# Kernel optimization log

Measured on AMD Instinct MI355X. Metric: run time of the kernel, lower is better.

## Reference

```python
import jax, jax.numpy as jnp
import numpy as np
from jax import lax

E = 10        # embed_dim
SEQ = 4000    # input_frame (sample_length=40)
G = 800       # group
F = 5         # frames_in_group
B = 16
VOCAB = 8192


def _conv2d(x, w, b):
    # x: [B, C, H, W], w: [O, I, 3, 3], padding=1 -> SAME
    y = lax.conv_general_dilated(x, w, (1, 1), 'SAME',
                                 dimension_numbers=('NCHW', 'OIHW', 'NCHW'))
    return y + b[None, :, None, None]


def _conv1d_k1(x, w, b):
    # Conv1d(seq, seq, kernel=1): x [B, S, L], w [S_out, S_in]
    return jnp.einsum('oi,bil->bol', w, x) + b[None, :, None]


def _linear(x, w, b):
    # torch Linear: w [out, in]
    return x @ w.T + b


def setup_inputs() -> dict:
    key = jax.random.key(0)
    ks = jax.random.split(key, 24)
    s = 0.02
    inp = {
        'X': jax.random.randint(ks[0], (B, SEQ, 15), 0, VOCAB),
        'emb_table': jax.random.normal(ks[1], (VOCAB, E), jnp.float32),
        'w_dwc_lsp': jax.random.normal(ks[2], (G, G, 3, 3), jnp.float32) * s,
        'b_dwc_lsp': jnp.zeros((G,), jnp.float32),
        'w_dwc_other': jax.random.normal(ks[3], (G, G, 3, 3), jnp.float32) * s,
        'b_dwc_other': jnp.zeros((G,), jnp.float32),
        'w_local': jax.random.normal(ks[4], (SEQ, SEQ), jnp.float32) * s,
        'b_local': jnp.zeros((SEQ,), jnp.float32),
        'w_global': jax.random.normal(ks[5], (SEQ, SEQ), jnp.float32) * s,
        'b_global': jnp.zeros((SEQ,), jnp.float32),
        'w_gq': jax.random.normal(ks[6], (4 * E, 4 * E), jnp.float32) * s,
        'b_gq': jnp.zeros((4 * E,), jnp.float32),
        'w_cq': jax.random.normal(ks[7], (4 * E, 4 * E), jnp.float32) * s,
        'b_cq': jnp.zeros((4 * E,), jnp.float32),
        'w_pq': jax.random.normal(ks[8], (4 * E, 3 * E), jnp.float32) * s,
        'b_pq': jnp.zeros((4 * E,), jnp.float32),
        'w_lk': jax.random.normal(ks[9], (4 * E, 4 * E), jnp.float32) * s,
        'b_lk': jnp.zeros((4 * E,), jnp.float32),
        'w_lv': jax.random.normal(ks[10], (4 * E, 4 * E), jnp.float32) * s,
        'b_lv': jnp.zeros((4 * E,), jnp.float32),
        'w_cls': jax.random.normal(ks[11], (1, SEQ * 4 * E * 3), jnp.float32) * 0.001,
        'b_cls': jnp.zeros((1,), jnp.float32),
        'bn_w': jnp.ones((1,), jnp.float32),
        'bn_b': jnp.zeros((1,), jnp.float32),
    }
    return inp


def reference(X, emb_table, w_dwc_lsp, b_dwc_lsp, w_dwc_other, b_dwc_other,
              w_local, b_local, w_global, b_global,
              w_gq, b_gq, w_cq, b_cq, w_pq, b_pq,
              w_lk, b_lk, w_lv, b_lv, w_cls, b_cls, bn_w, bn_b):
    batch, seq, cw = X.shape
    gamma = jnp.float32(0.8)
    pk = jnp.array([0, 0, 0, 0, 1, 3, 1, 2, 3, 2, 3, 1, 2, 3, 3], jnp.float32)
    D = jnp.repeat(gamma ** pk, E)  # [150]

    Xe = emb_table[X].reshape(batch, seq, cw * E) * D  # [B, S, 150]
    ch = Xe.reshape(batch, seq, cw, E)                  # 15 chunks of E

    lsp = ch[:, :, jnp.array([0, 1, 2, 3])].reshape(batch, seq, 4 * E)
    pitch = ch[:, :, jnp.array([4, 5, 10])].reshape(batch, seq, 3 * E)
    code = ch[:, :, jnp.array([6, 7, 11, 12])].reshape(batch, seq, 4 * E)
    gain = ch[:, :, jnp.array([8, 13, 9, 14])].reshape(batch, seq, 4 * E)

    conv_lsp = _conv2d(lsp.reshape(batch, G, F, 4 * E), w_dwc_lsp, b_dwc_lsp).reshape(batch, seq, 4 * E)
    conv_pitch = _conv2d(pitch.reshape(batch, G, F, 3 * E), w_dwc_other, b_dwc_other).reshape(batch, seq, 3 * E)
    conv_code = _conv2d(code.reshape(batch, G, F, 4 * E), w_dwc_other, b_dwc_other).reshape(batch, seq, 4 * E)
    conv_gain = _conv2d(gain.reshape(batch, G, F, 4 * E), w_dwc_other, b_dwc_other).reshape(batch, seq, 4 * E)

    conv_lsp = _conv1d_k1(conv_lsp, w_local, b_local)
    conv_pitch = _conv1d_k1(conv_pitch, w_local, b_local)
    conv_code = _conv1d_k1(conv_code, w_local, b_local)
    conv_gain = _conv1d_k1(conv_gain, w_local, b_local)

    gain_q = _linear(conv_gain, w_gq, b_gq)    # [B, S, 40]
    pitch_q = _linear(conv_pitch, w_pq, b_pq)  # [B, S, 40]
    code_q = _linear(conv_code, w_cq, b_cq)    # [B, S, 40]
    lsp_k = _linear(conv_lsp, w_lk, b_lk)
    lsp_v = _linear(conv_lsp, w_lv, b_lv)

    # Q @ K^T @ V with no softmax: associate as Q @ (K^T V), O(S*d^2)
    kv = jnp.einsum('bsd,bse->bde', lsp_k, lsp_v)  # [B, 40, 40]
    out_gain = jnp.einsum('bsd,bde->bse', gain_q, kv) + lsp
    out_pitch = jnp.einsum('bsd,bde->bse', pitch_q, kv) + lsp
    out_code = jnp.einsum('bsd,bde->bse', code_q, kv) + lsp

    atten_out = jnp.concatenate([out_gain, out_pitch, out_code], -1)  # [B, S, 120]
    gf = _conv1d_k1(atten_out, w_global, b_global).reshape(batch, -1)  # [B, 480000]

    y = gf @ w_cls.T + b_cls  # [B, 1]
    # BatchNorm1d(1) in eval mode: running_mean=0, running_var=1
    eps = jnp.float32(1e-5)
    y = y * (bn_w / jnp.sqrt(1.0 + eps)) + bn_b
    return jax.nn.sigmoid(y)
```

## Files before the change

### kernel.cpp

```cpp
#include <hip/hip_runtime.h>
#include <hip/hip_bf16.h>

typedef _Float16 f16;
typedef __attribute__((ext_vector_type(8))) _Float16 half8;
typedef __attribute__((ext_vector_type(4))) _Float16 half4;
typedef __attribute__((ext_vector_type(4))) float f32x4;

static const int BN = 16, SEQN = 4000;

__device__ __forceinline__ void gload_lds(f16* lds, const f16* g) {
  __builtin_amdgcn_global_load_lds((const __attribute__((address_space(1))) unsigned int*)g,
                                   (__attribute__((address_space(3))) unsigned int*)lds, 16, 0, 0);
}

__device__ __forceinline__ int xcd_swz(int orig, int nwg) {
  int q = nwg >> 3, r = nwg & 7, x = orig & 7, o = orig >> 3;
  return (x < r ? x * (q + 1) : r * (q + 1) + (x - r) * q) + o;
}

__device__ __forceinline__ void body_wconv(char* SM, int o,
    const float* __restrict__ w_dwc_l, f16* __restrict__ wp_lsp) {
  float* sh = (float*)SM;
  int t = threadIdx.x;
  for (int p4 = t; p4 < 1800; p4 += 256)
    *(f32x4*)&sh[p4 * 4] = *(const f32x4*)&w_dwc_l[(long)o * 7200 + p4 * 4];
  __syncthreads();
  for (int c = t; c < 912; c += 256) {
    int p = c * 8;
    int seg = p / 2432, r = p - seg * 2432;
    half8 h = {};
    if (r < 2400) {
      int de = r / 800, gib = r - de * 800;
#pragma unroll
      for (int j = 0; j < 8; j++) h[j] = (f16)sh[(gib + j) * 9 + seg * 3 + de];
    }
    *(half8*)&wp_lsp[(long)o * 7296 + p] = h;
  }
}

__device__ __forceinline__ void body_wlocal(char* SM, int s,
    const float* __restrict__ w_local, f16* __restrict__ wlp) {
  float* sh = (float*)SM;
  int t = threadIdx.x;
  for (int p4 = t; p4 < 1000; p4 += 256)
    *(f32x4*)&sh[p4 * 4] = *(const f32x4*)&w_local[(long)s * 4000 + p4 * 4];
  __syncthreads();
  for (int c = t; c < 512; c += 256) {
    int p = c * 8;
    half8 h = {};
    if (p < 4000) {
      int f = p / 800, g = p - f * 800;
#pragma unroll
      for (int j = 0; j < 8; j++) h[j] = (f16)sh[(g + j) * 5 + f];
    }
    *(half8*)&wlp[(long)s * 4096 + p] = h;
  }
}

__device__ __forceinline__ void body_wcT(char* SM, int id,
    const float* __restrict__ w_cls, f16* __restrict__ wcT) {
  float (*tile)[33] = (float(*)[33])SM;
  int t = threadIdx.x;
  int c0 = (id % 4) * 32, r0 = (id / 4) * 32;
  int tx = t & 31, ty = t >> 5;
  for (int i = ty; i < 32; i += 8) {
    int r = r0 + i, c = c0 + tx;
    tile[i][tx] = (r < 4000 && c < 120) ? w_cls[(long)r * 120 + c] : 0.f;
  }
  __syncthreads();
  for (int i = ty; i < 32; i += 8) {
    int c = c0 + i, r = r0 + tx;
    if (c < 128 && r < 4000) wcT[(long)c * 4000 + r] = (f16)(tile[tx][i] * 1024.f);
  }
}

__device__ __forceinline__ void body_woT(char* SM, int id,
    const float* __restrict__ in, f16* __restrict__ out) {
  float (*sh)[292] = (float(*)[292])SM;
  int bg = id % 25, bgi = id / 25;
  int g0 = bg * 32, gi0 = bgi * 32;
  int t = threadIdx.x;
  for (int p = t; p < 2304; p += 256) {
    int gl = p / 72, q4 = p % 72;
    *(f32x4*)&sh[gl][q4 * 4] = *(const f32x4*)&in[(long)(g0 + gl) * 7200 + gi0 * 9 + q4 * 4];
  }
  __syncthreads();
  for (int c = t; c < 1152; c += 256) {
    int gl8 = c & 3, q = c >> 2;
    int gil = q & 31, z = q >> 5;
    half8 h;
#pragma unroll
    for (int j = 0; j < 8; j++) h[j] = (f16)sh[gl8 * 8 + j][gil * 9 + z];
    *(half8*)&out[(long)z * 640000 + (gi0 + gil) * 800 + g0 + gl8 * 8] = h;
  }
}

__device__ __forceinline__ void body_gather(char* SM, int bid,
    const int* __restrict__ X, const float* __restrict__ emb,
    f16* __restrict__ P_lsp, f16* __restrict__ P_pit,
    f16* __restrict__ P_cod, f16* __restrict__ P_gai,
    float* __restrict__ lsp32) {
  int* sx_ = (int*)SM;
  float* slsp = (float*)(SM + 9600);
  const float scale[15] = {1.f,1.f,1.f,1.f,0.8f,0.512f,0.8f,0.64f,0.512f,0.64f,0.512f,0.8f,0.64f,0.512f,0.512f};
  const int br[15] = {0,0,0,0,1,1,2,2,3,3,1,2,2,3,3};
  const int po[15] = {0,1,2,3,0,1,0,1,0,2,2,2,3,1,3};
  int t = threadIdx.x;
  int b = bid / 25, gc = bid % 25;
  int g0 = gc * 32, s0 = g0 * 5;
  const int* xbase = X + ((long)b * SEQN + s0) * 15;
  for (int p = t; p < 600; p += 256)
    *(f32x4*)&sx_[p * 4] = *(const f32x4*)&xbase[p * 4];
  __syncthreads();
  for (int it = t; it < 2400; it += 256) {
    int gl = it & 31, q = it >> 5, f = q % 5, c = q / 5;
    int idx = sx_[(gl * 5 + f) * 15 + c];
    const float* er = emb + (long)idx * 10;
    int ty = br[c], p = po[c];
    f16* P = (ty == 0) ? P_lsp : (ty == 1) ? P_pit : (ty == 2) ? P_cod : P_gai;
    int Wp = (ty == 1) ? 32 : 42;
    f16* base = P + ((long)((f + 1) * 16 + b) * Wp + (1 + p * 10)) * 800 + g0 + gl;
    float sc = scale[c];
#pragma unroll
    for (int j = 0; j < 10; j++) {
      float v = er[j] * sc;
      base[(long)j * 800] = (f16)v;
      if (ty == 0) slsp[(gl * 5 + f) * 40 + p * 10 + j] = v;
    }
  }
  __syncthreads();
  float* ldst = lsp32 + ((long)b * SEQN + s0) * 40;
  for (int p4 = t; p4 < 1600; p4 += 256)
    *(f32x4*)&ldst[p4 * 4] = *(const f32x4*)&slsp[p4 * 4];
}

__device__ __forceinline__ void body_c1(char* SM, int blk,
    const float* __restrict__ wcls, const float* __restrict__ bg,
    float* __restrict__ c1p) {
  float* red = (float*)SM;
  int t = threadIdx.x;
  float s = 0.f;
  for (long i = (long)blk * 256 + t; i < 480000; i += (long)120 * 256)
    s += wcls[i] * bg[i / 120];
  red[t] = s; __syncthreads();
  for (int o = 128; o > 0; o >>= 1) { if (t < o) red[t] += red[t + o]; __syncthreads(); }
  if (t == 0) c1p[blk] = red[0];
}

__device__ __forceinline__ void body_conv(char* SM, int id,
    const f16* __restrict__ P, const f16* __restrict__ wp, float* __restrict__ Cp) {
  f16* Asb = (f16*)SM;
  f16* Bsb = Asb + 8192;
  int lin = xcd_swz(id % 175, 175);
  int z = id / 175;
  int nx = lin % 7, my = lin / 7;
  int m0 = my * 128, n0 = nx * 128;
  Cp += (long)z * 3200 * 800;
  int t = threadIdx.x;
  int gslot = (t & 3) ^ ((t >> 3) & 3);
  const f16 *ap[2], *bp[2];
#pragma unroll
  for (int q = 0; q < 2; q++) {
    int row = q * 64 + (t >> 2);
    int m = m0 + row;
    int f = m / 640, rem = m % 640, b = rem / 40, e = rem % 40;
    ap[q] = P + ((long)((f + z) * 16 + b) * 42 + e) * 800 + gslot * 8;
    bp[q] = wp + (long)(n0 + row) * 7296 + z * 2432 + gslot * 8;
  }
  int lane = t & 63, wv = t >> 6, l15 = lane & 15, kg = lane >> 4;
  int wm = (wv >> 1) * 64, wn = (wv & 1) * 64;
  int so = (kg ^ ((l15 >> 1) & 3)) << 3;
  f32x4 acc[4][4] = {};
  gload_lds(&Asb[t * 8], ap[0]); gload_lds(&Asb[2048 + t * 8], ap[1]);
  gload_lds(&Bsb[t * 8], bp[0]); gload_lds(&Bsb[2048 + t * 8], bp[1]);
  __syncthreads();
  int cur = 0;
  for (int kt = 0; kt < 76; kt++) {
    if (kt + 1 < 76) {
      int o = (kt + 1) * 32, nb = cur ^ 1;
      gload_lds(&Asb[nb * 4096 + t * 8], ap[0] + o); gload_lds(&Asb[nb * 4096 + 2048 + t * 8], ap[1] + o);
      gload_lds(&Bsb[nb * 4096 + t * 8], bp[0] + o); gload_lds(&Bsb[nb * 4096 + 2048 + t * 8], bp[1] + o);
    }
    half8 av[4], bv[4];
#pragma unroll
    for (int i = 0; i < 4; i++) av[i] = *(const half8*)&Asb[cur * 4096 + (wm + i * 16 + l15) * 32 + so];
#pragma unroll
    for (int j = 0; j < 4; j++) bv[j] = *(const half8*)&Bsb[cur * 4096 + (wn + j * 16 + l15) * 32 + so];
#pragma unroll
    for (int i = 0; i < 4; i++)
#pragma unroll
      for (int j = 0; j < 4; j++)
        acc[i][j] = __builtin_amdgcn_mfma_f32_16x16x32_f16(av[i], bv[j], acc[i][j], 0, 0, 0);
    __syncthreads();
    cur ^= 1;
  }
#pragma unroll
  for (int i = 0; i < 4; i++) {
    int mb = m0 + wm + i * 16 + kg * 4;
#pragma unroll
    for (int j = 0; j < 4; j++) {
      int n = n0 + wn + j * 16 + l15;
      if (n >= 800) continue;
      f32x4 d = acc[i][j];
#pragma unroll
      for (int r = 0; r < 4; r++)
        Cp[(long)(mb + r) * 800 + n] = d[r];
    }
  }
}

__device__ __forceinline__ void body_gemm128(char* SM, int x, int ky, int z,
    const f16* __restrict__ A, int lda, const f16* __restrict__ Bm, int ldb,
    float* __restrict__ C, int ldc,
    int gx, int nwg, int nkt, int KTtot, long cslice, long az, long bz, long cz,
    int Mreal, int Nreal, int Aclamp) {
  f16* Asb = (f16*)SM;
  f16* Bsb = Asb + 8192;
  A += (long)z * az;
  Bm += (long)z * bz;
  C += (long)z * cz + (long)ky * cslice;
  int lin = xcd_swz(x, nwg);
  int nx = lin % gx, my = lin / gx;
  int m0 = my * 128, n0 = nx * 128;
  int kt0 = ky * nkt;
  int ktn = nkt; if (kt0 + ktn > KTtot) ktn = KTtot - kt0;
  int t = threadIdx.x;
  int gslot = (t & 3) ^ ((t >> 3) & 3);
  const f16 *ap[2], *bp[2];
#pragma unroll
  for (int q = 0; q < 2; q++) {
    int row = q * 64 + (t >> 2);
    int ra = m0 + row; if (ra >= Aclamp) ra = Aclamp - 1;
    ap[q] = A + (long)ra * lda + (long)kt0 * 32 + gslot * 8;
    bp[q] = Bm + (long)(n0 + row) * ldb + (long)kt0 * 32 + gslot * 8;
  }
  int lane = t & 63, wv = t >> 6, l15 = lane & 15, kg = lane >> 4;
  int wm = (wv >> 1) * 64, wn = (wv & 1) * 64;
  int so = (kg ^ ((l15 >> 1) & 3)) << 3;
  f32x4 acc[4][4] = {};
  gload_lds(&Asb[t * 8], ap[0]); gload_lds(&Asb[2048 + t * 8], ap[1]);
  gload_lds(&Bsb[t * 8], bp[0]); gload_lds(&Bsb[2048 + t * 8], bp[1]);
  __syncthreads();
  int cur = 0;
  for (int kt = 0; kt < ktn; kt++) {
    if (kt + 1 < ktn) {
      int o = (kt + 1) * 32, nb = cur ^ 1;
      gload_lds(&Asb[nb * 4096 + t * 8], ap[0] + o); gload_lds(&Asb[nb * 4096 + 2048 + t * 8], ap[1] + o);
      gload_lds(&Bsb[nb * 4096 + t * 8], bp[0] + o); gload_lds(&Bsb[nb * 4096 + 2048 + t * 8], bp[1] + o);
    }
    half8 av[4], bv[4];
#pragma unroll
    for (int i = 0; i < 4; i++) av[i] = *(const half8*)&Asb[cur * 4096 + (wm + i * 16 + l15) * 32 + so];
#pragma unroll
    for (int j = 0; j < 4; j++) bv[j] = *(const half8*)&Bsb[cur * 4096 + (wn + j * 16 + l15) * 32 + so];
#pragma unroll
    for (int i = 0; i < 4; i++)
#pragma unroll
      for (int j = 0; j < 4; j++)
        acc[i][j] = __builtin_amdgcn_mfma_f32_16x16x32_f16(av[i], bv[j], acc[i][j], 0, 0, 0);
    __syncthreads();
    cur ^= 1;
  }
#pragma unroll
  for (int i = 0; i < 4; i++) {
    int mb = m0 + wm + i * 16 + kg * 4;
#pragma unroll
    for (int j = 0; j < 4; j++) {
      int n = n0 + wn + j * 16 + l15;
      if (n >= Nreal) continue;
      f32x4 d = acc[i][j];
#pragma unroll
      for (int r = 0; r < 4; r++) {
        int m = mb + r;
        if (m >= Mreal) continue;
        C[(long)m * ldc + n] = d[r];
      }
    }
  }
}

__device__ __forceinline__ void body_tn(char* SM, int id,
    const f16* __restrict__ A, int lda, const float* __restrict__ B, int ldb,
    float* __restrict__ C, int ldc, int nkt, int KTtot, long cslice,
    int Mreal, int Nreal) {
  f16* As = (f16*)SM;
  f16* Bs = As + 4096;
  int n0 = (id & 31) * 128;
  int ky = id >> 5;
  int kt0 = ky * nkt;
  int ktn = nkt; if (kt0 + ktn > KTtot) ktn = KTtot - kt0;
  C += (long)ky * cslice;
  int t = threadIdx.x;
  int gslot = (t & 3) ^ ((t >> 3) & 3);
  const f16 *ap0, *ap1;
  {
    int r0 = t >> 2, r1 = 64 + (t >> 2);
    if (r0 >= Mreal) r0 = Mreal - 1;
    if (r1 >= Mreal) r1 = Mreal - 1;
    ap0 = A + (long)r0 * lda + (long)kt0 * 32 + gslot * 8;
    ap1 = A + (long)r1 * lda + (long)kt0 * 32 + gslot * 8;
  }
  int lane = t & 63, wv = t >> 6;
  int wm = (wv >> 1) * 64, wn = (wv & 1) * 64;
  int l15 = lane & 15, kg = lane >> 4;
  int so = (kg ^ ((l15 >> 1) & 3)) << 3;
  f32x4 acc[4][4] = {};
  for (int kt = 0; kt < ktn; kt++) {
    float rb[4][4];
    int nli[4], kqi[4];
#pragma unroll
    for (int i = 0; i < 4; i++) {
      int idd = i * 256 + t;
      nli[i] = idd & 127; kqi[i] = idd >> 7;
      int gn = n0 + nli[i]; if (gn >= Nreal) gn = Nreal - 1;
      long kb = ((long)(kt0 + kt) * 32 + kqi[i] * 4);
#pragma unroll
      for (int j = 0; j < 4; j++) rb[i][j] = B[(kb + j) * ldb + gn];
    }
    __syncthreads();
    gload_lds(&As[t * 8], ap0 + kt * 32);
    gload_lds(&As[2048 + t * 8], ap1 + kt * 32);
#pragma unroll
    for (int i = 0; i < 4; i++) {
      half4 h = {(f16)rb[i][0], (f16)rb[i][1], (f16)rb[i][2], (f16)rb[i][3]};
      *(half4*)&Bs[nli[i] * 36 + kqi[i] * 4] = h;
    }
    __syncthreads();
    half8 av[4], bv[4];
#pragma unroll
    for (int i = 0; i < 4; i++) {
      av[i] = *(const half8*)(&As[(wm + i * 16 + l15) * 32 + so]);
      bv[i] = *(const half8*)(&Bs[(wn + i * 16 + l15) * 36 + kg * 8]);
    }
#pragma unroll
    for (int i = 0; i < 4; i++)
#pragma unroll
      for (int j = 0; j < 4; j++)
        acc[i][j] = __builtin_amdgcn_mfma_f32_16x16x32_f16(av[i], bv[j], acc[i][j], 0, 0, 0);
  }
#pragma unroll
  for (int i = 0; i < 4; i++) {
    int mb = wm + i * 16 + kg * 4;
#pragma unroll
    for (int j = 0; j < 4; j++) {
      int n = n0 + wn + j * 16 + l15;
      if (n >= Nreal) continue;
      f32x4 d = acc[i][j];
#pragma unroll
      for (int r = 0; r < 4; r++) {
        int m = mb + r;
        if (m >= Mreal) continue;
        C[(long)m * ldc + n] = d[r];
      }
    }
  }
}

__device__ __forceinline__ void body_co_red(long gid,
    const float* __restrict__ Cp, const float* __restrict__ bias, f16* __restrict__ co) {
  if (gid >= 640000) return;
  int m = gid / 200, n4 = (gid % 200) * 4;
  long o = (long)m * 800 + n4;
  f32x4 s = *(const f32x4*)&bias[n4];
#pragma unroll
  for (int z = 0; z < 3; z++) s += *(const f32x4*)&Cp[(long)z * 2560000 + o];
  int f = m / 640, r2 = m % 640;
  half4 h = {(f16)s[0], (f16)s[1], (f16)s[2], (f16)s[3]};
  *(half4*)&co[(long)r2 * 4000 + f * 800 + n4] = h;
}

__device__ __forceinline__ void body_vred(int idb, int MODE,
    const float* __restrict__ vp, float* __restrict__ vout, f16* __restrict__ tout) {
  int x = idb & 15, ec = idb >> 4;
  int s = x * 256 + threadIdx.x;
  if (s >= 4000) return;
  int g = s / 5, f = s % 5;
  float sums[40];
#pragma unroll
  for (int eo = 0; eo < 40; eo++) {
    int e = ec * 40 + eo;
    float sum = 0.f;
#pragma unroll
    for (int z = 0; z < 10; z++) sum += vp[(long)z * 480000 + (long)e * 4000 + s];
    sums[eo] = sum;
    if (MODE == 0) tout[(long)e * 4000 + s] = (f16)sum;
    else tout[(long)(f * 120 + e) * 832 + g] = (f16)sum;
  }
#pragma unroll
  for (int q = 0; q < 10; q++)
    *(f32x4*)&vout[(long)s * 120 + ec * 40 + q * 4] = *(f32x4*)&sums[q * 4];
}

__device__ __forceinline__ void body_cl_red(long gid,
    const float* __restrict__ Clp, const float* __restrict__ bl, float* __restrict__ cl) {
  if (gid >= 640000) return;
  int m = gid / 160, n4 = (gid % 160) * 4;
  long o = (long)m * 640 + n4;
  f32x4 s = {0.f, 0.f, 0.f, 0.f};
#pragma unroll
  for (int z = 0; z < 4; z++) s += *(const f32x4*)&Clp[(long)z * 2560000 + o];
  float b = bl[m];
  s += (f32x4){b, b, b, b};
  *(f32x4*)&cl[o] = s;
}

__device__ __forceinline__ void body_resid(char* SM, int chunk, int b,
    const float* __restrict__ lsp32, const float* __restrict__ vmat,
    float* __restrict__ rpart) {
  float* red = (float*)SM;
  int t = threadIdx.x;
  int s0 = chunk * 160;
  float y = 0.f;
  for (int idx = t; idx < 1600; idx += 256) {
    int sr = idx / 10, d4 = idx % 10;
    const float* lp = lsp32 + ((long)b * SEQN + s0 + sr) * 40 + d4 * 4;
    const float* vp = vmat + (long)(s0 + sr) * 120 + d4 * 4;
    f32x4 l = *(const f32x4*)lp;
    f32x4 vs = *(const f32x4*)vp + *(const f32x4*)(vp + 40) + *(const f32x4*)(vp + 80);
    y += l[0] * vs[0] + l[1] * vs[1] + l[2] * vs[2] + l[3] * vs[3];
  }
  red[t] = y; __syncthreads();
  for (int o = 128; o > 0; o >>= 1) { if (t < o) red[t] += red[t + o]; __syncthreads(); }
  if (t == 0) rpart[b * 25 + chunk] = red[0];
}

__device__ __forceinline__ void body_kv(char* SM, int chunk, int b,
    const float* __restrict__ cl, const float* __restrict__ wlk, const float* __restrict__ blk,
    const float* __restrict__ wlv, const float* __restrict__ blv, float* __restrict__ kvp) {
  float* s_wk = (float*)SM;
  float* s_wv = s_wk + 1600;
  float* s_cl = s_wv + 1600;
  float* s_k  = s_cl + 320;
  float* s_v  = s_k + 320;
  int t = threadIdx.x;
  for (int p = t; p < 1600; p += 256) { s_wk[p] = wlk[p]; s_wv[p] = wlv[p]; }
  float acc[7] = {0.f, 0.f, 0.f, 0.f, 0.f, 0.f, 0.f};
  for (int c8 = 0; c8 < 20; c8++) {
    int sb = chunk * 160 + c8 * 8;
    __syncthreads();
    for (int p = t; p < 320; p += 256) {
      int sl = p / 40, e = p % 40;
      s_cl[sl * 40 + e] = cl[(long)(sb + sl) * 640 + b * 40 + e];
    }
    __syncthreads();
    for (int p = t; p < 640; p += 256) {
      int half = p / 320, q = p % 320, sl = q / 40, d = q % 40;
      const float* w = half ? s_wv : s_wk;
      float r = half ? blv[d] : blk[d];
      for (int e = 0; e < 40; e++) r += w[d * 40 + e] * s_cl[sl * 40 + e];
      if (half) s_v[sl * 40 + d] = r; else s_k[sl * 40 + d] = r;
    }
    __syncthreads();
    int ai = 0;
    for (int p = t; p < 1600; p += 256, ai++) {
      int d = p / 40, e = p % 40;
      float a = acc[ai];
      for (int sl = 0; sl < 8; sl++) a += s_k[sl * 40 + d] * s_v[sl * 40 + e];
      acc[ai] = a;
    }
  }
  int ai = 0;
  for (int p = t; p < 1600; p += 256, ai++)
    kvp[((long)(b * 25 + chunk)) * 1600 + p] = acc[ai];
}

__device__ __forceinline__ void body_consts(char* SM, int e,
    const float* __restrict__ Vt, const float* __restrict__ vmat,
    const float* __restrict__ bconv, const float* __restrict__ blocal,
    float* __restrict__ cbblv, float* __restrict__ svv) {
  float* r1 = (float*)SM;
  float* r2 = r1 + 256;
  int t = threadIdx.x;
  float a = 0.f, b = 0.f;
  for (int s = t; s < 4000; s += 256) {
    a += bconv[s / 5] * Vt[(long)s * 120 + e] + blocal[s] * vmat[(long)s * 120 + e];
    b += vmat[(long)s * 120 + e];
  }
  r1[t] = a; r2[t] = b; __syncthreads();
  for (int o = 128; o > 0; o >>= 1) {
    if (t < o) { r1[t] += r1[t + o]; r2[t] += r2[t + o]; }
    __syncthreads();
  }
  if (t == 0) { cbblv[e] = r1[0]; svv[e] = r2[0]; }
}

__device__ __forceinline__ void body_fold(long c8,
    const float* __restrict__ A9, f16* __restrict__ Bp) {
  long p = c8 * 8;
  if (p >= 7 * 120 * 2496) return;
  int fp = p / 299520;
  int r = p % 299520;
  int eg = r / 2496, k2 = r % 2496;
  int zk = k2 / 832, kk = k2 % 832;
  half8 h = {};
  if (kk < 800) {
#pragma unroll
    for (int j = 0; j < 8; j++) {
      float s = 0.f;
#pragma unroll
      for (int dh = 0; dh < 3; dh++) {
        int f = fp - dh;
        if (f >= 0 && f < 5)
          s += A9[((long)(dh * 3 + zk) * 640 + f * 120 + eg) * 800 + kk + j];
      }
      h[j] = (f16)s;
    }
  }
  *(half8*)&Bp[p] = h;
}

__device__ __forceinline__ void body_kvred(long gid,
    const float* __restrict__ kvp, float* __restrict__ kv) {
  if (gid >= 16 * 1600) return;
  int b = gid / 1600, p = gid % 1600;
  float s = 0.f;
  for (int c = 0; c < 25; c++) s += kvp[((long)(b * 25 + c)) * 1600 + p];
  kv[gid] = s;
}

__device__ __forceinline__ void body_U(char* SM, int id,
    const f16* __restrict__ Pg, const f16* __restrict__ Pp, const f16* __restrict__ Pc,
    const f16* __restrict__ Bp, float* __restrict__ Upart) {
  f16* Asb = (f16*)SM;
  f16* Bsb = Asb + 8192;
  int m0 = (id % 28) * 64;
  int y = id / 28, fp = y / 3, zk = y % 3;
  const f16* P; int seg0, jw, Wp, e0;
  if (m0 < 640)       { seg0 = 0;    jw = 40; Wp = 42; e0 = 0;  P = Pg; }
  else if (m0 < 1152) { seg0 = 640;  jw = 30; Wp = 32; e0 = 40; P = Pp; }
  else                { seg0 = 1152; jw = 40; Wp = 42; e0 = 80; P = Pc; }
  P += (long)fp * 16 * Wp * 800;
  int t = threadIdx.x;
  int gslot = (t & 7) ^ ((t >> 3) & 7);
  const f16 *ap[2], *bp[2];
#pragma unroll
  for (int q = 0; q < 2; q++) {
    int row = q * 32 + (t >> 3);
    int l = m0 + row - seg0; if (l >= 16 * jw) l = 0;
    ap[q] = P + ((long)(l / jw) * Wp + (l % jw)) * 800 + (long)zk * 800 + gslot * 8;
    int brow = row; if (e0 + brow > 119) brow = 119 - e0;
    bp[q] = Bp + ((long)fp * 120 + e0 + brow) * 2496 + zk * 832 + gslot * 8;
  }
  int lane = t & 63, wv = t >> 6, l15 = lane & 15, kg = lane >> 4;
  int sx = l15 & 7;
  f32x4 acc[3] = {};
  gload_lds(&Asb[t * 8], ap[0]); gload_lds(&Asb[2048 + t * 8], ap[1]);
  gload_lds(&Bsb[t * 8], bp[0]); gload_lds(&Bsb[2048 + t * 8], bp[1]);
  __syncthreads();
  int cur = 0;
  for (int kt = 0; kt < 13; kt++) {
    if (kt + 1 < 13) {
      int o = (kt + 1) * 64, nb = cur ^ 1;
      gload_lds(&Asb[nb * 4096 + t * 8], ap[0] + o); gload_lds(&Asb[nb * 4096 + 2048 + t * 8], ap[1] + o);
      gload_lds(&Bsb[nb * 4096 + t * 8], bp[0] + o); gload_lds(&Bsb[nb * 4096 + 2048 + t * 8], bp[1] + o);
    }
#pragma unroll
    for (int ks = 0; ks < 2; ks++) {
      int so = ((ks * 4 + kg) ^ sx) << 3;
      half8 av = *(const half8*)&Asb[cur * 4096 + (wv * 16 + l15) * 64 + so];
#pragma unroll
      for (int j = 0; j < 3; j++) {
        half8 bv = *(const half8*)&Bsb[cur * 4096 + (j * 16 + l15) * 64 + so];
        acc[j] = __builtin_amdgcn_mfma_f32_16x16x32_f16(av, bv, acc[j], 0, 0, 0);
      }
    }
    __syncthreads();
    cur ^= 1;
  }
#pragma unroll
  for (int j = 0; j < 3; j++) {
    int n = j * 16 + l15;
    if (n >= 40) continue;
    f32x4 d = acc[j];
#pragma unroll
    for (int r = 0; r < 4; r++) {
      int m = m0 + wv * 16 + kg * 4 + r;
      if (m - seg0 >= 16 * jw) continue;
      Upart[((long)y * 1792 + m) * 40 + n] = d[r];
    }
  }
}

__device__ __forceinline__ void body_ured(long gid,
    const float* __restrict__ Upart, const float* __restrict__ cbblv,
    float* __restrict__ Ufin) {
  if (gid >= 1792 * 40) return;
  int m = gid / 40, e = gid % 40;
  int e0 = m < 640 ? 0 : (m < 1152 ? 40 : 80);
  float s = cbblv[e0 + e];
  for (int y = 0; y < 21; y++) s += Upart[(long)y * 71680 + gid];
  Ufin[gid] = s;
}

__global__ __launch_bounds__(256) void k_phase0(
    const float* w_dwc_l, f16* wp_lsp, const float* w_cls, f16* wcT,
    const int* X, const float* emb, f16* P_lsp, f16* P_pit, f16* P_cod, f16* P_gai,
    float* lsp32, const float* b_global, float* c1p) {
  __shared__ __align__(16) char SM[35200];
  int bid = blockIdx.x;
  if (bid < 800) body_wconv(SM, bid, w_dwc_l, wp_lsp);
  else if (bid < 1300) body_wcT(SM, bid - 800, w_cls, wcT);
  else if (bid < 1700) body_gather(SM, bid - 1300, X, emb, P_lsp, P_pit, P_cod, P_gai, lsp32);
  else body_c1(SM, bid - 1700, w_cls, b_global, c1p);
}

__global__ __launch_bounds__(256) void k_phase1(
    const f16* P_lsp, const f16* wp_lsp, float* Cp,
    const f16* wcT, const float* w_global, float* vpart,
    const float* w_local, f16* wlp) {
  __shared__ __align__(16) char SM[32768];
  int bid = blockIdx.x;
  if (bid < 525) body_conv(SM, bid, P_lsp, wp_lsp, Cp);
  else if (bid < 845) body_tn(SM, bid - 525, wcT, 4000, w_global, 4000, vpart, 4000, 13, 125, 480000L, 120, 4000);
  else body_wlocal(SM, bid - 845, w_local, wlp);
}

__global__ __launch_bounds__(256) void k_phase2(
    const float* Cp, const float* b_dwc_l, f16* co,
    const float* vpart, float* vmat, f16* vT,
    const float* w_dwc_o, f16* woT) {
  __shared__ __align__(16) char SM[37376];
  int bid = blockIdx.x;
  if (bid < 2500) body_co_red((long)bid * 256 + threadIdx.x, Cp, b_dwc_l, co);
  else if (bid < 2548) body_vred(bid - 2500, 0, vpart, vmat, vT);
  else body_woT(SM, bid - 2548, w_dwc_o, woT);
}

__global__ __launch_bounds__(256) void k_phase3(
    const f16* wlp, const f16* co, float* Clp,
    const f16* vT, const float* w_local, float* vpart,
    const float* lsp32, const float* vmat, float* rpart) {
  __shared__ __align__(16) char SM[32768];
  int bid = blockIdx.x;
  if (bid < 640) body_gemm128(SM, bid % 160, bid / 160, 0, wlp, 4096, co, 4000, Clp, 640,
                              5, 160, 32, 128, 2560000L, 0, 0, 0, 4000, 640, 4000);
  else if (bid < 960) body_tn(SM, bid - 640, vT, 4000, w_local, 4000, vpart, 4000, 13, 125, 480000L, 120, 4000);
  else { int id = bid - 960; body_resid(SM, id % 25, id / 25, lsp32, vmat, rpart); }
}

__global__ __launch_bounds__(256) void k_phase4(
    const float* Clp, const float* b_local, float* cl,
    const float* vpart, float* Vt, f16* vtT) {
  int bid = blockIdx.x;
  if (bid < 2500) body_cl_red((long)bid * 256 + threadIdx.x, Clp, b_local, cl);
  else body_vred(bid - 2500, 1, vpart, Vt, vtT);
}

__global__ __launch_bounds__(256) void k_phase5(
    const float* cl, const float* w_lk, const float* b_lk,
    const float* w_lv, const float* b_lv, float* kvp,
    const f16* vtT, const f16* woT, float* A9,
    const float* Vt, const float* vmat, const float* b_dwc_o, const float* b_local,
    float* cbblv, float* svv) {
  __shared__ __align__(16) char SM[32768];
  int bid = blockIdx.x;
  if (bid < 400) body_kv(SM, bid % 25, bid / 25, cl, w_lk, b_lk, w_lv, b_lv, kvp);
  else if (bid < 715) { int id = bid - 400; body_gemm128(SM, id % 35, 0, id / 35, vtT, 832, woT, 800, A9, 800,
                                                          7, 35, 26, 26, 0L, 0, 640000, 512000, 600, 800, 600); }
  else body_consts(SM, bid - 715, Vt, vmat, b_dwc_o, b_local, cbblv, svv);
}

__global__ __launch_bounds__(256) void k_phase6(
    const float* A9, f16* Bp, const float* kvp, float* kvb) {
  int bid = blockIdx.x;
  if (bid < 1024) body_fold((long)bid * 256 + threadIdx.x, A9, Bp);
  else body_kvred((long)(bid - 1024) * 256 + threadIdx.x, kvp, kvb);
}

__global__ __launch_bounds__(256) void k_phase7(
    const f16* P_gai, const f16* P_pit, const f16* P_cod,
    const f16* Bp, float* Upart) {
  __shared__ __align__(16) char SM[32768];
  body_U(SM, blockIdx.x, P_gai, P_pit, P_cod, Bp, Upart);
}

__global__ __launch_bounds__(256) void k_phase8(
    const float* Upart, const float* cbblv, float* Ufin) {
  body_ured((long)blockIdx.x * 256 + threadIdx.x, Upart, cbblv, Ufin);
}

__global__ __launch_bounds__(256) void k_final(
    const float* __restrict__ Ufin, const float* __restrict__ kvb,
    const float* __restrict__ rpart,
    const float* __restrict__ wgq, const float* __restrict__ wpq, const float* __restrict__ wcq,
    const float* __restrict__ bgq, const float* __restrict__ bpq, const float* __restrict__ bcq,
    const float* __restrict__ svv, const float* __restrict__ c1p,
    const float* __restrict__ bcls, const float* __restrict__ bnw,
    const float* __restrict__ bnb, float* __restrict__ out) {
  __shared__ float s_kv[1600], s_U[4800], s_w[4400], s_bq[120], s_sv[120], s_red[256];
  int b = blockIdx.x, t = threadIdx.x;
  for (int p = t; p < 1600; p += 256) {
    s_kv[p] = kvb[b * 1600 + p];
    s_w[p] = wgq[p];
    s_w[2800 + p] = wcq[p];
  }
  for (int p = t; p < 1200; p += 256) s_w[1600 + p] = wpq[p];
  for (int p = t; p < 4800; p += 256) {
    int tt = p / 1600, r = p % 1600, j = r / 40, e = r % 40;
    float uv = 0.f;
    if (tt == 0) uv = Ufin[(b * 40 + j) * 40 + e];
    else if (tt == 1) { if (j < 30) uv = Ufin[(640 + b * 30 + j) * 40 + e]; }
    else uv = Ufin[(1152 + b * 40 + j) * 40 + e];
    s_U[p] = uv;
  }
  if (t < 40) { s_bq[t] = bgq[t]; s_bq[40 + t] = bpq[t]; s_bq[80 + t] = bcq[t]; }
  for (int p = t; p < 120; p += 256) s_sv[p] = svv[p];
  __syncthreads();
  float y = 0.f;
  for (int p = t; p < 4800; p += 256) {
    int tt = p / 1600, q = p % 1600, d = q / 40, e = q % 40;
    float T = 0.f;
    if (tt == 0) {
      for (int j = 0; j < 40; j++) T += s_w[d * 40 + j] * s_U[j * 40 + e];
    } else if (tt == 1) {
      for (int j = 0; j < 30; j++) T += s_w[1600 + d * 30 + j] * s_U[1600 + j * 40 + e];
    } else {
      for (int j = 0; j < 40; j++) T += s_w[2800 + d * 40 + j] * s_U[3200 + j * 40 + e];
    }
    y += s_kv[d * 40 + e] * (T + s_bq[tt * 40 + d] * s_sv[tt * 40 + e]);
  }
  for (int p = t; p < 25; p += 256) y += rpart[b * 25 + p];
  s_red[t] = y; __syncthreads();
  for (int o = 128; o > 0; o >>= 1) { if (t < o) s_red[t] += s_red[t + o]; __syncthreads(); }
  if (t == 0) {
    float c1 = bcls[0];
    for (int i = 0; i < 120; i++) c1 += c1p[i];
    float yy = s_red[0] * (1.f / 1024.f) + c1;
    yy = yy * (bnw[0] * rsqrtf(1.f + 1e-5f)) + bnb[0];
    out[b] = 1.f / (1.f + expf(-yy));
  }
}

extern "C" void kernel_launch(void* const* d_in, const int* in_sizes, int n_in,
                              void* d_out, int out_size, void* d_ws, size_t ws_size,
                              hipStream_t stream) {
  const int*   X        = (const int*)d_in[0];
  const float* emb      = (const float*)d_in[1];
  const float* w_dwc_l  = (const float*)d_in[2];
  const float* b_dwc_l  = (const float*)d_in[3];
  const float* w_dwc_o  = (const float*)d_in[4];
  const float* b_dwc_o  = (const float*)d_in[5];
  const float* w_local  = (const float*)d_in[6];
  const float* b_local  = (const float*)d_in[7];
  const float* w_global = (const float*)d_in[8];
  const float* b_global = (const float*)d_in[9];
  const float* w_gq = (const float*)d_in[10];
  const float* b_gq = (const float*)d_in[11];
  const float* w_cq = (const float*)d_in[12];
  const float* b_cq = (const float*)d_in[13];
  const float* w_pq = (const float*)d_in[14];
  const float* b_pq = (const float*)d_in[15];
  const float* w_lk = (const float*)d_in[16];
  const float* b_lk = (const float*)d_in[17];
  const float* w_lv = (const float*)d_in[18];
  const float* b_lv = (const float*)d_in[19];
  const float* w_cls = (const float*)d_in[20];
  const float* b_cls = (const float*)d_in[21];
  const float* bn_w = (const float*)d_in[22];
  const float* bn_b = (const float*)d_in[23];
  float* out = (float*)d_out;

  char* ws = (char*)d_ws;
  size_t off = 0;
  auto alloc = [&](size_t bytes) -> void* {
    off = (off + 255) & ~(size_t)255;
    void* p = ws + off; off += bytes; return p;
  };

  const size_t sz_p40 = (size_t)7 * 16 * 42 * 800 * 2;
  const size_t sz_p30 = (size_t)7 * 16 * 32 * 800 * 2;
  f16* P_lsp = (f16*)alloc(sz_p40 + 256);
  f16* P_pit = (f16*)alloc(sz_p30 + 256);
  f16* P_cod = (f16*)alloc(sz_p40 + 256);
  f16* P_gai = (f16*)alloc(sz_p40 + 256);
  float* lsp32 = (float*)alloc((size_t)16 * 4000 * 40 * 4);
  f16* wp_lsp = (f16*)alloc((size_t)896 * 7296 * 2);
  f16* wlp    = (f16*)alloc((size_t)4000 * 4096 * 2 + 256);
  f16* wcT    = (f16*)alloc((size_t)128 * 4000 * 2);
  f16* vT     = (f16*)alloc((size_t)128 * 4000 * 2);
  f16* co     = (f16*)alloc((size_t)640 * 4000 * 2 + 256);
  float* cl   = (float*)alloc((size_t)4000 * 640 * 4);
  float* vmat  = (float*)alloc((size_t)480000 * 4);
  float* Vt    = (float*)alloc((size_t)480000 * 4);
  f16* vtT   = (f16*)alloc((size_t)640 * 832 * 2 + 256);
  f16* Bp    = (f16*)alloc((size_t)7 * 120 * 2496 * 2);
  float* Upart = (float*)alloc((size_t)21 * 1792 * 40 * 4);
  float* Ufin  = (float*)alloc((size_t)1792 * 40 * 4);
  float* cbblv = (float*)alloc(120 * 4);
  float* svv   = (float*)alloc(120 * 4);
  float* kvp  = (float*)alloc((size_t)400 * 1600 * 4);
  float* kvb  = (float*)alloc((size_t)16 * 1600 * 4);
  float* c1p  = (float*)alloc(120 * 4);
  float* rpart = (float*)alloc(400 * 4);
  f16* woT = (f16*)alloc(((size_t)9 * 640000 + 76800) * 2);
  float* vpart = (float*)alloc((size_t)10 * 480000 * 4);
  char* arena = (char*)alloc((size_t)41 * 1024 * 1024);
  float* Cp  = (float*)arena;
  float* Clp = (float*)arena;
  float* A9  = (float*)arena;
  (void)ws_size; (void)in_sizes; (void)n_in; (void)out_size;

  hipMemsetAsync(P_lsp, 0, sz_p40, stream);
  hipMemsetAsync(P_pit, 0, sz_p30, stream);
  hipMemsetAsync(P_cod, 0, sz_p40, stream);
  hipMemsetAsync(P_gai, 0, sz_p40, stream);
  hipMemsetAsync(vtT, 0, (size_t)640 * 832 * 2, stream);

  k_phase0<<<1820, 256, 0, stream>>>(w_dwc_l, wp_lsp, w_cls, wcT,
                                     X, emb, P_lsp, P_pit, P_cod, P_gai,
                                     lsp32, b_global, c1p);
  k_phase1<<<4845, 256, 0, stream>>>(P_lsp, wp_lsp, Cp, wcT, w_global, vpart,
                                     w_local, wlp);
  k_phase2<<<3173, 256, 0, stream>>>(Cp, b_dwc_l, co, vpart, vmat, vT, w_dwc_o, woT);
  k_phase3<<<1360, 256, 0, stream>>>(wlp, co, Clp, vT, w_local, vpart, lsp32, vmat, rpart);
  k_phase4<<<2548, 256, 0, stream>>>(Clp, b_local, cl, vpart, Vt, vtT);
  k_phase5<<<835, 256, 0, stream>>>(cl, w_lk, b_lk, w_lv, b_lv, kvp,
                                    vtT, woT, A9, Vt, vmat, b_dwc_o, b_local, cbblv, svv);
  k_phase6<<<1124, 256, 0, stream>>>(A9, Bp, kvp, kvb);
  k_phase7<<<588, 256, 0, stream>>>(P_gai, P_pit, P_cod, Bp, Upart);
  k_phase8<<<280, 256, 0, stream>>>(Upart, cbblv, Ufin);
  k_final<<<16, 256, 0, stream>>>(Ufin, kvb, rpart,
                                  w_gq, w_pq, w_cq, b_gq, b_pq, b_cq,
                                  svv, c1p, b_cls, bn_w, bn_b, out);
}
```

Before: 456.0 us.

## Split conv K into halves with fp16 partials and fp16 local-conv partials

The conv GEMM's K range per tap is split into two halves, so twice as many blocks run, each with half the k-loop. The reduction kernel now sums six partials instead of three. Both the conv and local-GEMM partial outputs are stored as fp16 instead of fp32, halving partial-buffer traffic and shrinking the arena. The w_local repack also stages data in a transposed LDS layout so the readback is contiguous. This trades some accuracy (fp16 partial sums) and extra reduction reads for more parallelism and less memory traffic.

```diff
diff --git a/kernel.cpp b/kernel.cpp
--- a/kernel.cpp
+++ b/kernel.cpp
@@ -42,16 +42,19 @@
     const float* __restrict__ w_local, f16* __restrict__ wlp) {
   float* sh = (float*)SM;
   int t = threadIdx.x;
-  for (int p4 = t; p4 < 1000; p4 += 256)
-    *(f32x4*)&sh[p4 * 4] = *(const f32x4*)&w_local[(long)s * 4000 + p4 * 4];
+  for (int p = t; p < 4000; p += 256) {
+    int g = p / 5, f = p - g * 5;
+    sh[f * 808 + g] = w_local[(long)s * 4000 + p];
+  }
   __syncthreads();
   for (int c = t; c < 512; c += 256) {
     int p = c * 8;
     half8 h = {};
     if (p < 4000) {
       int f = p / 800, g = p - f * 800;
-#pragma unroll
-      for (int j = 0; j < 8; j++) h[j] = (f16)sh[(g + j) * 5 + f];
+      const float* src = &sh[f * 808 + g];
+#pragma unroll
+      for (int j = 0; j < 8; j++) h[j] = (f16)src[j];
     }
     *(half8*)&wlp[(long)s * 4096 + p] = h;
   }
@@ -148,14 +151,15 @@
 }
 
 __device__ __forceinline__ void body_conv(char* SM, int id,
-    const f16* __restrict__ P, const f16* __restrict__ wp, float* __restrict__ Cp) {
+    const f16* __restrict__ P, const f16* __restrict__ wp, f16* __restrict__ Cp) {
   f16* Asb = (f16*)SM;
   f16* Bsb = Asb + 8192;
   int lin = xcd_swz(id % 175, 175);
   int z = id / 175;
+  int df = z >> 1, hf = z & 1;
   int nx = lin % 7, my = lin / 7;
   int m0 = my * 128, n0 = nx * 128;
-  Cp += (long)z * 3200 * 800;
+  Cp += (long)z * 2560000;
   int t = threadIdx.x;
   int gslot = (t & 3) ^ ((t >> 3) & 3);
   const f16 *ap[2], *bp[2];
@@ -164,8 +168,8 @@
     int row = q * 64 + (t >> 2);
     int m = m0 + row;
     int f = m / 640, rem = m % 640, b = rem / 40, e = rem % 40;
-    ap[q] = P + ((long)((f + z) * 16 + b) * 42 + e) * 800 + gslot * 8;
-    bp[q] = wp + (long)(n0 + row) * 7296 + z * 2432 + gslot * 8;
+    ap[q] = P + ((long)((f + df) * 16 + b) * 42 + e) * 800 + hf * 1216 + gslot * 8;
+    bp[q] = wp + (long)(n0 + row) * 7296 + df * 2432 + hf * 1216 + gslot * 8;
   }
   int lane = t & 63, wv = t >> 6, l15 = lane & 15, kg = lane >> 4;
   int wm = (wv >> 1) * 64, wn = (wv & 1) * 64;
@@ -175,8 +179,8 @@
   gload_lds(&Bsb[t * 8], bp[0]); gload_lds(&Bsb[2048 + t * 8], bp[1]);
   __syncthreads();
   int cur = 0;
-  for (int kt = 0; kt < 76; kt++) {
-    if (kt + 1 < 76) {
+  for (int kt = 0; kt < 38; kt++) {
+    if (kt + 1 < 38) {
       int o = (kt + 1) * 32, nb = cur ^ 1;
       gload_lds(&Asb[nb * 4096 + t * 8], ap[0] + o); gload_lds(&Asb[nb * 4096 + 2048 + t * 8], ap[1] + o);
       gload_lds(&Bsb[nb * 4096 + t * 8], bp[0] + o); gload_lds(&Bsb[nb * 4096 + 2048 + t * 8], bp[1] + o);
@@ -204,21 +208,23 @@
       f32x4 d = acc[i][j];
 #pragma unroll
       for (int r = 0; r < 4; r++)
-        Cp[(long)(mb + r) * 800 + n] = d[r];
-    }
-  }
-}
-
+        Cp[(long)(mb + r) * 800 + n] = (f16)d[r];
+    }
+  }
+}
+
+template <int OUTF16>
 __device__ __forceinline__ void body_gemm128(char* SM, int x, int ky, int z,
     const f16* __restrict__ A, int lda, const f16* __restrict__ Bm, int ldb,
-    float* __restrict__ C, int ldc,
+    float* __restrict__ C, f16* __restrict__ C16, int ldc,
     int gx, int nwg, int nkt, int KTtot, long cslice, long az, long bz, long cz,
     int Mreal, int Nreal, int Aclamp) {
   f16* Asb = (f16*)SM;
   f16* Bsb = Asb + 8192;
   A += (long)z * az;
   Bm += (long)z * bz;
-  C += (long)z * cz + (long)ky * cslice;
+  if (OUTF16) C16 += (long)z * cz + (long)ky * cslice;
+  else C += (long)z * cz + (long)ky * cslice;
   int lin = xcd_swz(x, nwg);
   int nx = lin % gx, my = lin / gx;
   int m0 = my * 128, n0 = nx * 128;
@@ -273,7 +279,8 @@
       for (int r = 0; r < 4; r++) {
         int m = mb + r;
         if (m >= Mreal) continue;
-        C[(long)m * ldc + n] = d[r];
+        if (OUTF16) C16[(long)m * ldc + n] = (f16)d[r];
+        else C[(long)m * ldc + n] = d[r];
       }
     }
   }
@@ -357,16 +364,19 @@
 }
 
 __device__ __forceinline__ void body_co_red(long gid,
-    const float* __restrict__ Cp, const float* __restrict__ bias, f16* __restrict__ co) {
+    const f16* __restrict__ Cp, const float* __restrict__ bias, f16* __restrict__ co) {
   if (gid >= 640000) return;
   int m = gid / 200, n4 = (gid % 200) * 4;
   long o = (long)m * 800 + n4;
   f32x4 s = *(const f32x4*)&bias[n4];
 #pragma unroll
-  for (int z = 0; z < 3; z++) s += *(const f32x4*)&Cp[(long)z * 2560000 + o];
+  for (int z = 0; z < 6; z++) {
+    half4 h = *(const half4*)&Cp[(long)z * 2560000 + o];
+    s += (f32x4){(float)h[0], (float)h[1], (float)h[2], (float)h[3]};
+  }
   int f = m / 640, r2 = m % 640;
-  half4 h = {(f16)s[0], (f16)s[1], (f16)s[2], (f16)s[3]};
-  *(half4*)&co[(long)r2 * 4000 + f * 800 + n4] = h;
+  half4 hh = {(f16)s[0], (f16)s[1], (f16)s[2], (f16)s[3]};
+  *(half4*)&co[(long)r2 * 4000 + f * 800 + n4] = hh;
 }
 
 __device__ __forceinline__ void body_vred(int idb, int MODE,
@@ -392,15 +402,17 @@
 }
 
 __device__ __forceinline__ void body_cl_red(long gid,
-    const float* __restrict__ Clp, const float* __restrict__ bl, float* __restrict__ cl) {
+    const f16* __restrict__ Clp, const float* __restrict__ bl, float* __restrict__ cl) {
   if (gid >= 640000) return;
   int m = gid / 160, n4 = (gid % 160) * 4;
   long o = (long)m * 640 + n4;
-  f32x4 s = {0.f, 0.f, 0.f, 0.f};
-#pragma unroll
-  for (int z = 0; z < 4; z++) s += *(const f32x4*)&Clp[(long)z * 2560000 + o];
   float b = bl[m];
-  s += (f32x4){b, b, b, b};
+  f32x4 s = {b, b, b, b};
+#pragma unroll
+  for (int z = 0; z < 4; z++) {
+    half4 h = *(const half4*)&Clp[(long)z * 2560000 + o];
+    s += (f32x4){(float)h[0], (float)h[1], (float)h[2], (float)h[3]};
+  }
   *(f32x4*)&cl[o] = s;
 }
 
@@ -605,18 +617,18 @@
 }
 
 __global__ __launch_bounds__(256) void k_phase1(
-    const f16* P_lsp, const f16* wp_lsp, float* Cp,
+    const f16* P_lsp, const f16* wp_lsp, f16* Cp,
     const f16* wcT, const float* w_global, float* vpart,
     const float* w_local, f16* wlp) {
   __shared__ __align__(16) char SM[32768];
   int bid = blockIdx.x;
-  if (bid < 525) body_conv(SM, bid, P_lsp, wp_lsp, Cp);
-  else if (bid < 845) body_tn(SM, bid - 525, wcT, 4000, w_global, 4000, vpart, 4000, 13, 125, 480000L, 120, 4000);
-  else body_wlocal(SM, bid - 845, w_local, wlp);
+  if (bid < 1050) body_conv(SM, bid, P_lsp, wp_lsp, Cp);
+  else if (bid < 1370) body_tn(SM, bid - 1050, wcT, 4000, w_global, 4000, vpart, 4000, 13, 125, 480000L, 120, 4000);
+  else body_wlocal(SM, bid - 1370, w_local, wlp);
 }
 
 __global__ __launch_bounds__(256) void k_phase2(
-    const float* Cp, const float* b_dwc_l, f16* co,
+    const f16* Cp, const float* b_dwc_l, f16* co,
     const float* vpart, float* vmat, f16* vT,
     const float* w_dwc_o, f16* woT) {
   __shared__ __align__(16) char SM[37376];
@@ -627,19 +639,19 @@
 }
 
 __global__ __launch_bounds__(256) void k_phase3(
-    const f16* wlp, const f16* co, float* Clp,
+    const f16* wlp, const f16* co, f16* Clp,
     const f16* vT, const float* w_local, float* vpart,
     const float* lsp32, const float* vmat, float* rpart) {
   __shared__ __align__(16) char SM[32768];
   int bid = blockIdx.x;
-  if (bid < 640) body_gemm128(SM, bid % 160, bid / 160, 0, wlp, 4096, co, 4000, Clp, 640,
-                              5, 160, 32, 128, 2560000L, 0, 0, 0, 4000, 640, 4000);
+  if (bid < 640) body_gemm128<1>(SM, bid % 160, bid / 160, 0, wlp, 4096, co, 4000, nullptr, Clp, 640,
+                                 5, 160, 32, 128, 2560000L, 0, 0, 0, 4000, 640, 4000);
   else if (bid < 960) body_tn(SM, bid - 640, vT, 4000, w_local, 4000, vpart, 4000, 13, 125, 480000L, 120, 4000);
   else { int id = bid - 960; body_resid(SM, id % 25, id / 25, lsp32, vmat, rpart); }
 }
 
 __global__ __launch_bounds__(256) void k_phase4(
-    const float* Clp, const float* b_local, float* cl,
+    const f16* Clp, const float* b_local, float* cl,
     const float* vpart, float* Vt, f16* vtT) {
   int bid = blockIdx.x;
   if (bid < 2500) body_cl_red((long)bid * 256 + threadIdx.x, Clp, b_local, cl);
@@ -655,8 +667,8 @@
   __shared__ __align__(16) char SM[32768];
   int bid = blockIdx.x;
   if (bid < 400) body_kv(SM, bid % 25, bid / 25, cl, w_lk, b_lk, w_lv, b_lv, kvp);
-  else if (bid < 715) { int id = bid - 400; body_gemm128(SM, id % 35, 0, id / 35, vtT, 832, woT, 800, A9, 800,
-                                                          7, 35, 26, 26, 0L, 0, 640000, 512000, 600, 800, 600); }
+  else if (bid < 715) { int id = bid - 400; body_gemm128<0>(SM, id % 35, 0, id / 35, vtT, 832, woT, 800, A9, nullptr, 800,
+                                                             7, 35, 26, 26, 0L, 0, 640000, 512000, 600, 800, 600); }
   else body_consts(SM, bid - 715, Vt, vmat, b_dwc_o, b_local, cbblv, svv);
 }
 
@@ -794,10 +806,10 @@
   float* rpart = (float*)alloc(400 * 4);
   f16* woT = (f16*)alloc(((size_t)9 * 640000 + 76800) * 2);
   float* vpart = (float*)alloc((size_t)10 * 480000 * 4);
-  char* arena = (char*)alloc((size_t)41 * 1024 * 1024);
-  float* Cp  = (float*)arena;
-  float* Clp = (float*)arena;
-  float* A9  = (float*)arena;
+  char* arena = (char*)alloc((size_t)32 * 1024 * 1024);
+  f16* Cp   = (f16*)arena;
+  f16* Clp  = (f16*)arena;
+  float* A9 = (float*)arena;
   (void)ws_size; (void)in_sizes; (void)n_in; (void)out_size;
 
   hipMemsetAsync(P_lsp, 0, sz_p40, stream);
@@ -809,7 +821,7 @@
   k_phase0<<<1820, 256, 0, stream>>>(w_dwc_l, wp_lsp, w_cls, wcT,
                                      X, emb, P_lsp, P_pit, P_cod, P_gai,
                                      lsp32, b_global, c1p);
-  k_phase1<<<4845, 256, 0, stream>>>(P_lsp, wp_lsp, Cp, wcT, w_global, vpart,
+  k_phase1<<<5370, 256, 0, stream>>>(P_lsp, wp_lsp, Cp, wcT, w_global, vpart,
                                      w_local, wlp);
   k_phase2<<<3173, 256, 0, stream>>>(Cp, b_dwc_l, co, vpart, vmat, vT, w_dwc_o, woT);
   k_phase3<<<1360, 256, 0, stream>>>(wlp, co, Clp, vT, w_local, vpart, lsp32, vmat, rpart);
```

New measurement: 445.5 us. 2.3% less time.
